# Kernel optimization log

Hardware: AMD Instinct MI355X
Metric: run time of the kernel (lower is better)

Reference implementation:

```python
import jax, jax.numpy as jnp
import numpy as np

T, B, I, H, O = 4096, 256, 64, 36, 2


def setup_inputs() -> dict:
    key = jax.random.key(0)
    ks = jax.random.split(key, 7)
    s = 1.0 / np.sqrt(H)  # PyTorch LSTM init scale
    return {
        "x": jax.random.normal(ks[0], (T, B, I), dtype=jnp.float32),
        "W_ih": jax.random.uniform(ks[1], (4 * H, I), minval=-s, maxval=s, dtype=jnp.float32),
        "W_hh": jax.random.uniform(ks[2], (4 * H, H), minval=-s, maxval=s, dtype=jnp.float32),
        "b_ih": jax.random.uniform(ks[3], (4 * H,), minval=-s, maxval=s, dtype=jnp.float32),
        "b_hh": jax.random.uniform(ks[4], (4 * H,), minval=-s, maxval=s, dtype=jnp.float32),
        "W_out": jax.random.uniform(ks[5], (O, H), minval=-s, maxval=s, dtype=jnp.float32),
        "b_out": jax.random.uniform(ks[6], (O,), minval=-s, maxval=s, dtype=jnp.float32),
    }


def reference(x, W_ih, W_hh, b_ih, b_hh, W_out, b_out):
    # Precompute input contribution for all timesteps in one big GEMM: [T,B,4H]
    xg = jnp.einsum("tbi,gi->tbg", x, W_ih) + (b_ih + b_hh)
    h0 = jnp.zeros((x.shape[1], H), dtype=x.dtype)
    c0 = jnp.zeros((x.shape[1], H), dtype=x.dtype)

    def step(carry, xg_t):
        h, c = carry
        gates = xg_t + h @ W_hh.T  # [B, 4H]
        i_g, f_g, g_g, o_g = jnp.split(gates, 4, axis=-1)  # PyTorch gate order i,f,g,o
        i_g = jax.nn.sigmoid(i_g)
        f_g = jax.nn.sigmoid(f_g)
        g_g = jnp.tanh(g_g)
        o_g = jax.nn.sigmoid(o_g)
        c = f_g * c + i_g * g_g
        h = o_g * jnp.tanh(c)
        return (h, c), h

    _, hs = jax.lax.scan(step, (h0, c0), xg)  # hs: [T, B, H]
    y = jnp.einsum("tbh,oh->tbo", hs, W_out) + b_out
    return y
```

## Files before the change

### kernel.cpp

```cpp
#include <hip/hip_runtime.h>
#include <hip/hip_fp16.h>

#define B_ 256
#define T_ 4096
#define I_ 64
#define H_ 36
#define G_ 144
#define O_ 2
#define TS 32
#define NTILES (T_ / TS)
#define UNROLL 8

typedef __fp16 h2 __attribute__((ext_vector_type(2)));

__device__ __forceinline__ float fsigmoid(float x) {
  float e = __builtin_amdgcn_exp2f(x * -1.442695040888963f);
  return __builtin_amdgcn_rcpf(1.0f + e);
}
__device__ __forceinline__ float ftanh(float x) {
  float e = __builtin_amdgcn_exp2f(x * 2.885390081777926f);
  return 1.0f - 2.0f * __builtin_amdgcn_rcpf(1.0f + e);
}
__device__ __forceinline__ h2 pack2(float lo, float hi) {
  return __builtin_amdgcn_cvt_pkrtz(lo, hi);
}
__device__ __forceinline__ float fdot2(h2 a, h2 b, float c) {
  return __builtin_amdgcn_fdot2(a, b, c, false);
}

__device__ __forceinline__ int pack_pair_dpp(float v) {
  int n_i = __builtin_amdgcn_update_dpp(0, __float_as_int(v), 0xF5, 0xF, 0xF, true);
  return __builtin_bit_cast(int, pack2(v, __int_as_float(n_i)));
}

__global__ __launch_bounds__(192, 1) void lstm_fused(
    const float* __restrict__ x,
    const float* __restrict__ W_ih,
    const float* __restrict__ W_hh,
    const float* __restrict__ b_ih,
    const float* __restrict__ b_hh,
    const float* __restrict__ W_out,
    const float* __restrict__ b_out,
    float* __restrict__ y)
{
  __shared__ float buf[2][TS * G_];
  __shared__ float ybuf[2][TS][O_];

  const int b = blockIdx.x;
  const int tid = threadIdx.x;
  const int wv = tid >> 6;
  const int j = tid & 63;

  h2 wA[36], wB[36];
  float hj = 0.0f, cj = 0.0f, yb = 0.0f;
  int jj = 0;

  h2 wp0[32], wp1[32];
  float bias0 = 0.f, bias1 = 0.f;
  int rowA = 0, rowB = 0;
  bool hasB = false;

  if (wv == 0) {
    if (j < H_) {
#pragma unroll
      for (int t = 0; t < 18; t++) {
        wA[t]      = pack2(W_hh[j * H_ + 2 * t],            W_hh[j * H_ + 2 * t + 1]);
        wA[18 + t] = pack2(W_hh[(j + H_) * H_ + 2 * t],     W_hh[(j + H_) * H_ + 2 * t + 1]);
        wB[t]      = pack2(W_hh[(j + 2 * H_) * H_ + 2 * t], W_hh[(j + 2 * H_) * H_ + 2 * t + 1]);
        wB[18 + t] = pack2(W_hh[(j + 3 * H_) * H_ + 2 * t], W_hh[(j + 3 * H_) * H_ + 2 * t + 1]);
      }
    } else if (j < H_ + O_) {
      const int o = j - H_;
#pragma unroll
      for (int t = 0; t < 18; t++) {
        wA[t] = pack2(W_out[o * H_ + 2 * t], W_out[o * H_ + 2 * t + 1]);
        wA[18 + t] = pack2(0.f, 0.f);
        wB[t] = pack2(0.f, 0.f); wB[18 + t] = pack2(0.f, 0.f);
      }
      yb = b_out[o];
    } else {
#pragma unroll
      for (int k = 0; k < H_; k++) { wA[k] = pack2(0.f, 0.f); wB[k] = pack2(0.f, 0.f); }
    }
    jj = (j < H_) ? j : 0;
    __builtin_amdgcn_s_setprio(1);
  } else {
    const int base = (wv - 1) * 72;
    rowA = base + j;
    hasB = (j < 8);
    rowB = base + 64 + (j & 7);
#pragma unroll
    for (int k = 0; k < 32; k++) {
      wp0[k] = pack2(W_ih[rowA * I_ + 2 * k], W_ih[rowA * I_ + 2 * k + 1]);
      wp1[k] = hasB ? pack2(W_ih[rowB * I_ + 2 * k], W_ih[rowB * I_ + 2 * k + 1])
                    : pack2(0.f, 0.f);
    }
    bias0 = b_ih[rowA] + b_hh[rowA];
    bias1 = hasB ? (b_ih[rowB] + b_hh[rowB]) : 0.f;
  }

  auto produce = [&](int tt, float* dst) {
    const float* xcol = x + ((size_t)(tt * TS) * B_ + b) * I_ + j;
#pragma unroll 1
    for (int c4 = 0; c4 < TS / 4; ++c4) {
      float xv0 = xcol[(size_t)(c4 * 4 + 0) * (B_ * I_)];
      float xv1 = xcol[(size_t)(c4 * 4 + 1) * (B_ * I_)];
      float xv2 = xcol[(size_t)(c4 * 4 + 2) * (B_ * I_)];
      float xv3 = xcol[(size_t)(c4 * 4 + 3) * (B_ * I_)];
      float xa[4] = {xv0, xv1, xv2, xv3};
#pragma unroll
      for (int u = 0; u < 4; ++u) {
        const int s = c4 * 4 + u;
        int xp = pack_pair_dpp(xa[u]);
        float a0e = bias0, a0o = 0.f, a1e = bias1, a1o = 0.f;
#pragma unroll
        for (int k = 0; k < 32; k += 2) {
          h2 pe = __builtin_bit_cast(h2, __builtin_amdgcn_readlane(xp, 2 * k));
          h2 po = __builtin_bit_cast(h2, __builtin_amdgcn_readlane(xp, 2 * k + 2));
          a0e = fdot2(wp0[k], pe, a0e);
          a0o = fdot2(wp0[k + 1], po, a0o);
          a1e = fdot2(wp1[k], pe, a1e);
          a1o = fdot2(wp1[k + 1], po, a1o);
        }
        dst[s * G_ + rowA] = a0e + a0o;
        if (hasB) dst[s * G_ + rowB] = a1e + a1o;
      }
    }
  };

  if (wv >= 1) produce(0, &buf[0][0]);
  __syncthreads();

  for (int tile = 0; tile < NTILES; ++tile) {
    if (wv >= 1) {
      if (wv == 1 && tile >= 1) {
        const int tp = tile - 1;
        const int s = j >> 1, o = j & 1;
        const int gt = tp * TS + s - 1;
        float v = ybuf[tp & 1][s][o];
        if (gt >= 0) y[((size_t)gt * B_ + b) * O_ + o] = v;
      }
      if (tile + 1 < NTILES) produce(tile + 1, &buf[(tile + 1) & 1][0]);
    } else {
      const float* bp = &buf[tile & 1][0];
#pragma unroll 1
      for (int ch = 0; ch < TS / UNROLL; ++ch) {
        float xi[UNROLL], xf[UNROLL], xg_[UNROLL], xo[UNROLL];
#pragma unroll
        for (int k = 0; k < UNROLL; ++k) {
          const int s = ch * UNROLL + k;
          xi[k]  = bp[s * G_ + jj];
          xf[k]  = bp[s * G_ + 36 + jj];
          xg_[k] = bp[s * G_ + 72 + jj];
          xo[k]  = bp[s * G_ + 108 + jj];
        }

#pragma unroll
        for (int k = 0; k < UNROLL; ++k) {
          const int s = ch * UNROLL + k;

          int hpi = pack_pair_dpp(hj);
          int hb[18];
#pragma unroll
          for (int t = 0; t < 18; ++t) hb[t] = __builtin_amdgcn_readlane(hpi, 2 * t);

          float a_i0, a_f0, a_g0, a_o0;
          if (j < H_) {
            a_i0 = xi[k]; a_f0 = xf[k]; a_g0 = xg_[k]; a_o0 = xo[k];
          } else {
            a_i0 = yb; a_f0 = 0.f; a_g0 = 0.f; a_o0 = 0.f;
          }
          float a_i1 = 0.f, a_f1 = 0.f, a_g1 = 0.f, a_o1 = 0.f;
#pragma unroll
          for (int t = 0; t < 18; t += 2) {
            h2 hh0 = __builtin_bit_cast(h2, hb[t]);
            h2 hh1 = __builtin_bit_cast(h2, hb[t + 1]);
            a_i0 = fdot2(wA[t], hh0, a_i0);       a_i1 = fdot2(wA[t + 1], hh1, a_i1);
            a_f0 = fdot2(wA[18 + t], hh0, a_f0);  a_f1 = fdot2(wA[18 + t + 1], hh1, a_f1);
            a_g0 = fdot2(wB[t], hh0, a_g0);       a_g1 = fdot2(wB[t + 1], hh1, a_g1);
            a_o0 = fdot2(wB[18 + t], hh0, a_o0);  a_o1 = fdot2(wB[18 + t + 1], hh1, a_o1);
          }
          float a_i = a_i0 + a_i1;

          if (j < H_) {
            float ig = fsigmoid(a_i);
            float fg = fsigmoid(a_f0 + a_f1);
            float gg = ftanh(a_g0 + a_g1);
            float og = fsigmoid(a_o0 + a_o1);
            cj = fg * cj + ig * gg;
            hj = og * ftanh(cj);
          } else if (j < H_ + O_) {
            ybuf[tile & 1][s][j - H_] = a_i;
          }
        }
      }
    }
    __syncthreads();
  }

  if (wv == 1) {
    const int tp = NTILES - 1;
    const int s = j >> 1, o = j & 1;
    const int gt = tp * TS + s - 1;
    float v = ybuf[tp & 1][s][o];
    if (gt >= 0) y[((size_t)gt * B_ + b) * O_ + o] = v;
  } else if (wv == 0) {
    __builtin_amdgcn_s_setprio(0);
    int hpi = pack_pair_dpp(hj);
    float a = yb;
#pragma unroll
    for (int t = 0; t < 18; ++t) {
      h2 hh = __builtin_bit_cast(h2, __builtin_amdgcn_readlane(hpi, 2 * t));
      a = fdot2(wA[t], hh, a);
    }
    if (j == H_ || j == H_ + 1) {
      y[((size_t)(T_ - 1) * B_ + b) * O_ + (j - H_)] = a;
    }
  }
}

extern "C" void kernel_launch(void* const* d_in, const int* in_sizes, int n_in,
                              void* d_out, int out_size, void* d_ws, size_t ws_size,
                              hipStream_t stream) {
  const float* x     = (const float*)d_in[0];
  const float* W_ih  = (const float*)d_in[1];
  const float* W_hh  = (const float*)d_in[2];
  const float* b_ih  = (const float*)d_in[3];
  const float* b_hh  = (const float*)d_in[4];
  const float* W_out = (const float*)d_in[5];
  const float* b_out = (const float*)d_in[6];
  float* y           = (float*)d_out;

  lstm_fused<<<dim3(B_), dim3(192), 0, stream>>>(
      x, W_ih, W_hh, b_ih, b_hh, W_out, b_out, y);
}
```

Measured before the change: 1.265 ms.

## Interleave gate layout in LDS for float2 reads and double time tile size

Producer waves now write the precomputed input-gate values into shared memory interleaved as (i,f) and (g,o) pairs per hidden unit. The recurrent wave can then fetch them with two 8-byte LDS reads per step instead of four scalar reads. The time tile doubles from 32 to 64 steps, which halves the number of block-wide barriers, and the y writeback loops twice per wave to cover the larger tile. The cost is twice the shared memory for the double buffer, plus a longer pipeline prologue.

```diff
diff --git a/kernel.cpp b/kernel.cpp
--- a/kernel.cpp
+++ b/kernel.cpp
@@ -7,7 +7,7 @@
 #define H_ 36
 #define G_ 144
 #define O_ 2
-#define TS 32
+#define TS 64
 #define NTILES (T_ / TS)
 #define UNROLL 8
 
@@ -27,6 +27,7 @@
 __device__ __forceinline__ float fdot2(h2 a, h2 b, float c) {
   return __builtin_amdgcn_fdot2(a, b, c, false);
 }
+__device__ __forceinline__ h2 asH2(int v) { return __builtin_bit_cast(h2, v); }
 
 __device__ __forceinline__ int pack_pair_dpp(float v) {
   int n_i = __builtin_amdgcn_update_dpp(0, __float_as_int(v), 0xF5, 0xF, 0xF, true);
@@ -57,8 +58,13 @@
 
   h2 wp0[32], wp1[32];
   float bias0 = 0.f, bias1 = 0.f;
-  int rowA = 0, rowB = 0;
+  int offA = 0, offB = 0;
   bool hasB = false;
+
+  auto rowoff = [](int r) {
+    int g = r / 36, u = r - g * 36;
+    return ((g >> 1) ? 72 : 0) + u * 2 + (g & 1);
+  };
 
   if (wv == 0) {
     if (j < H_) {
@@ -86,9 +92,11 @@
     __builtin_amdgcn_s_setprio(1);
   } else {
     const int base = (wv - 1) * 72;
-    rowA = base + j;
+    const int rowA = base + j;
     hasB = (j < 8);
-    rowB = base + 64 + (j & 7);
+    const int rowB = base + 64 + (j & 7);
+    offA = rowoff(rowA);
+    offB = rowoff(rowB);
 #pragma unroll
     for (int k = 0; k < 32; k++) {
       wp0[k] = pack2(W_ih[rowA * I_ + 2 * k], W_ih[rowA * I_ + 2 * k + 1]);
@@ -103,11 +111,10 @@
     const float* xcol = x + ((size_t)(tt * TS) * B_ + b) * I_ + j;
 #pragma unroll 1
     for (int c4 = 0; c4 < TS / 4; ++c4) {
-      float xv0 = xcol[(size_t)(c4 * 4 + 0) * (B_ * I_)];
-      float xv1 = xcol[(size_t)(c4 * 4 + 1) * (B_ * I_)];
-      float xv2 = xcol[(size_t)(c4 * 4 + 2) * (B_ * I_)];
-      float xv3 = xcol[(size_t)(c4 * 4 + 3) * (B_ * I_)];
-      float xa[4] = {xv0, xv1, xv2, xv3};
+      float xa[4];
+#pragma unroll
+      for (int u = 0; u < 4; ++u)
+        xa[u] = xcol[(size_t)(c4 * 4 + u) * (B_ * I_)];
 #pragma unroll
       for (int u = 0; u < 4; ++u) {
         const int s = c4 * 4 + u;
@@ -115,15 +122,15 @@
         float a0e = bias0, a0o = 0.f, a1e = bias1, a1o = 0.f;
 #pragma unroll
         for (int k = 0; k < 32; k += 2) {
-          h2 pe = __builtin_bit_cast(h2, __builtin_amdgcn_readlane(xp, 2 * k));
-          h2 po = __builtin_bit_cast(h2, __builtin_amdgcn_readlane(xp, 2 * k + 2));
+          h2 pe = asH2(__builtin_amdgcn_readlane(xp, 2 * k));
+          h2 po = asH2(__builtin_amdgcn_readlane(xp, 2 * k + 2));
           a0e = fdot2(wp0[k], pe, a0e);
           a0o = fdot2(wp0[k + 1], po, a0o);
           a1e = fdot2(wp1[k], pe, a1e);
           a1o = fdot2(wp1[k + 1], po, a1o);
         }
-        dst[s * G_ + rowA] = a0e + a0o;
-        if (hasB) dst[s * G_ + rowB] = a1e + a1o;
+        dst[s * G_ + offA] = a0e + a0o;
+        if (hasB) dst[s * G_ + offB] = a1e + a1o;
       }
     }
   };
@@ -135,24 +142,26 @@
     if (wv >= 1) {
       if (wv == 1 && tile >= 1) {
         const int tp = tile - 1;
-        const int s = j >> 1, o = j & 1;
-        const int gt = tp * TS + s - 1;
-        float v = ybuf[tp & 1][s][o];
-        if (gt >= 0) y[((size_t)gt * B_ + b) * O_ + o] = v;
+#pragma unroll
+        for (int q = 0; q < 2; ++q) {
+          const int v = q * 64 + j;
+          const int s = v >> 1, o = v & 1;
+          const int gt = tp * TS + s - 1;
+          float vv = ybuf[tp & 1][s][o];
+          if (gt >= 0) y[((size_t)gt * B_ + b) * O_ + o] = vv;
+        }
       }
       if (tile + 1 < NTILES) produce(tile + 1, &buf[(tile + 1) & 1][0]);
     } else {
       const float* bp = &buf[tile & 1][0];
 #pragma unroll 1
       for (int ch = 0; ch < TS / UNROLL; ++ch) {
-        float xi[UNROLL], xf[UNROLL], xg_[UNROLL], xo[UNROLL];
+        float2 xif[UNROLL], xgo[UNROLL];
 #pragma unroll
         for (int k = 0; k < UNROLL; ++k) {
           const int s = ch * UNROLL + k;
-          xi[k]  = bp[s * G_ + jj];
-          xf[k]  = bp[s * G_ + 36 + jj];
-          xg_[k] = bp[s * G_ + 72 + jj];
-          xo[k]  = bp[s * G_ + 108 + jj];
+          xif[k] = *(const float2*)&bp[s * G_ + 2 * jj];
+          xgo[k] = *(const float2*)&bp[s * G_ + 72 + 2 * jj];
         }
 
 #pragma unroll
@@ -166,15 +175,16 @@
 
           float a_i0, a_f0, a_g0, a_o0;
           if (j < H_) {
-            a_i0 = xi[k]; a_f0 = xf[k]; a_g0 = xg_[k]; a_o0 = xo[k];
+            a_i0 = xif[k].x; a_f0 = xif[k].y;
+            a_g0 = xgo[k].x; a_o0 = xgo[k].y;
           } else {
             a_i0 = yb; a_f0 = 0.f; a_g0 = 0.f; a_o0 = 0.f;
           }
           float a_i1 = 0.f, a_f1 = 0.f, a_g1 = 0.f, a_o1 = 0.f;
 #pragma unroll
           for (int t = 0; t < 18; t += 2) {
-            h2 hh0 = __builtin_bit_cast(h2, hb[t]);
-            h2 hh1 = __builtin_bit_cast(h2, hb[t + 1]);
+            h2 hh0 = asH2(hb[t]);
+            h2 hh1 = asH2(hb[t + 1]);
             a_i0 = fdot2(wA[t], hh0, a_i0);       a_i1 = fdot2(wA[t + 1], hh1, a_i1);
             a_f0 = fdot2(wA[18 + t], hh0, a_f0);  a_f1 = fdot2(wA[18 + t + 1], hh1, a_f1);
             a_g0 = fdot2(wB[t], hh0, a_g0);       a_g1 = fdot2(wB[t + 1], hh1, a_g1);
@@ -200,18 +210,21 @@
 
   if (wv == 1) {
     const int tp = NTILES - 1;
-    const int s = j >> 1, o = j & 1;
-    const int gt = tp * TS + s - 1;
-    float v = ybuf[tp & 1][s][o];
-    if (gt >= 0) y[((size_t)gt * B_ + b) * O_ + o] = v;
+#pragma unroll
+    for (int q = 0; q < 2; ++q) {
+      const int v = q * 64 + j;
+      const int s = v >> 1, o = v & 1;
+      const int gt = tp * TS + s - 1;
+      float vv = ybuf[tp & 1][s][o];
+      if (gt >= 0) y[((size_t)gt * B_ + b) * O_ + o] = vv;
+    }
   } else if (wv == 0) {
     __builtin_amdgcn_s_setprio(0);
     int hpi = pack_pair_dpp(hj);
     float a = yb;
 #pragma unroll
     for (int t = 0; t < 18; ++t) {
-      h2 hh = __builtin_bit_cast(h2, __builtin_amdgcn_readlane(hpi, 2 * t));
-      a = fdot2(wA[t], hh, a);
+      a = fdot2(wA[t], asH2(__builtin_amdgcn_readlane(hpi, 2 * t)), a);
     }
     if (j == H_ || j == H_ + 1) {
       y[((size_t)(T_ - 1) * B_ + b) * O_ + (j - H_)] = a;
```

Result: no change. 1.274 ms (+0.8%).
